# Performance work log

Hardware: AMD Instinct MI355X
Metric: run time of the kernel (lower is better)

## Reference

```python
import jax, jax.numpy as jnp
import numpy as np

B, S, D, H = 2, 2048, 1024, 16
DK = D // H


def setup_inputs() -> dict:
    key = jax.random.key(0)
    ks = jax.random.split(key, 12)
    scale = 1.0 / np.sqrt(D)
    inp = {
        "q": jax.random.normal(ks[0], (B, S, D), jnp.float32),
        "k": jax.random.normal(ks[1], (B, S, D), jnp.float32),
        "v": jax.random.normal(ks[2], (B, S, D), jnp.float32),
        "mask": jax.random.randint(ks[3], (B, 1, S, S), 0, 2, jnp.int32),
        "w_q": jax.random.normal(ks[4], (D, D), jnp.float32) * scale,
        "b_q": jnp.zeros((D,), jnp.float32),
        "w_k": jax.random.normal(ks[5], (D, D), jnp.float32) * scale,
        "b_k": jnp.zeros((D,), jnp.float32),
        "w_v": jax.random.normal(ks[6], (D, D), jnp.float32) * scale,
        "b_v": jnp.zeros((D,), jnp.float32),
        "w_o": jax.random.normal(ks[7], (D, D), jnp.float32) * scale,
        "b_o": jnp.zeros((D,), jnp.float32),
    }
    return inp


def reference(q, k, v, mask, w_q, b_q, w_k, b_k, w_v, b_v, w_o, b_o):
    # linear projections (torch Linear: x @ W.T + b)
    qp = q @ w_q.T + b_q  # [B,S,D]
    kp = k @ w_k.T + b_k
    vp = v @ w_v.T + b_v
    # split heads -> [B,H,S,DK]
    qh = qp.reshape(B, S, H, DK).transpose(0, 2, 1, 3)
    kh = kp.reshape(B, S, H, DK).transpose(0, 2, 1, 3)
    vh = vp.reshape(B, S, H, DK).transpose(0, 2, 1, 3)
    # scaled dot-product attention
    scores = jnp.einsum("bhqd,bhkd->bhqk", qh, kh) / jnp.sqrt(jnp.float32(DK))
    scores = jnp.where(mask == 0, jnp.float32(-1e9), scores)
    attn = jax.nn.softmax(scores, axis=-1)
    ctx = jnp.einsum("bhqk,bhkd->bhqd", attn, vh)  # [B,H,S,DK]
    ctx = ctx.transpose(0, 2, 1, 3).reshape(B, S, D)
    return ctx @ w_o.T + b_o
```

## Files before the change

### kernel.cpp

```cpp
#include <hip/hip_runtime.h>
#include <hip/hip_bf16.h>
#include <cstdint>

#define DEVINL __device__ __forceinline__

using bfrag = __attribute__((ext_vector_type(8))) __bf16;
using f32x4 = __attribute__((ext_vector_type(4))) float;
using f32x16 = __attribute__((ext_vector_type(16))) float;
using u16x4 = __attribute__((ext_vector_type(4))) unsigned short;
using u16x8 = __attribute__((ext_vector_type(8))) unsigned short;
using u32x4 = __attribute__((ext_vector_type(4))) unsigned int;

static constexpr int S_ = 2048;
static constexpr int D_ = 1024;
static constexpr int MROWS = 4096;

DEVINL unsigned short f2bf(float f) {
  __hip_bfloat16 h = __float2bfloat16(f);
  union { __hip_bfloat16 h; unsigned short u; } cv; cv.h = h; return cv.u;
}

DEVINL float fexp2(float x) {
#if __has_builtin(__builtin_amdgcn_exp2f)
  return __builtin_amdgcn_exp2f(x);
#else
  return exp2f(x);
#endif
}

DEVINL unsigned cvtpk(float lo, float hi) {
  unsigned r;
  asm("v_cvt_pk_bf16_f32 %0, %1, %2" : "=v"(r) : "v"(lo), "v"(hi));
  return r;
}

DEVINL void plswap(unsigned& x, unsigned& y) {
#if __has_builtin(__builtin_amdgcn_permlane32_swap)
  auto r = __builtin_amdgcn_permlane32_swap(x, y, false, false);
  x = r[0]; y = r[1];
#else
  unsigned px = __shfl_xor(x, 32), py = __shfl_xor(y, 32);
  bool h = (threadIdx.x & 32) != 0;
  unsigned nx = h ? py : x;
  unsigned ny = h ? y : px;
  x = nx; y = ny;
#endif
}

DEVINL void async_copy16(void* lds, const void* g) {
  __builtin_amdgcn_global_load_lds(
      (const __attribute__((address_space(1))) unsigned int*)g,
      (__attribute__((address_space(3))) unsigned int*)lds, 16, 0, 0);
}

struct CvtAll {
  const float* src[7];
  unsigned short* dst[7];
  int n4[7];
  const int* mask;
  unsigned long long* bits;
  int nmask;
};

__global__ __launch_bounds__(256) void cvt_all(CvtAll a) {
  if (blockIdx.y == 7) {
    const int n = a.nmask;
    for (int i = blockIdx.x * 256 + threadIdx.x; i < n; i += gridDim.x * 256) {
      unsigned long long b = __ballot(a.mask[i] != 0);
      if ((threadIdx.x & 63) == 0) a.bits[i >> 6] = b;
    }
    return;
  }
  const float* __restrict__ in = a.src[blockIdx.y];
  unsigned short* __restrict__ out = a.dst[blockIdx.y];
  const int n4 = a.n4[blockIdx.y];
  for (int i = blockIdx.x * 256 + threadIdx.x; i < n4; i += gridDim.x * 256) {
    f32x4 v = ((const f32x4*)in)[i];
    u16x4 o;
    o[0] = f2bf(v[0]); o[1] = f2bf(v[1]); o[2] = f2bf(v[2]); o[3] = f2bf(v[3]);
    ((u16x4*)out)[i] = o;
  }
}

template <int OMODE>
DEVINL void gemm_body(const unsigned short* __restrict__ A, const unsigned short* __restrict__ W,
                      const float* __restrict__ bias, void* __restrict__ Cout,
                      int K, int N, float oscale,
                      unsigned short* As, unsigned short* Bs, int m0, int n0) {
  const int t = threadIdx.x;
  const int lane = t & 63, wave = t >> 6;
  const int wr = wave >> 1, wc = wave & 1;
  const int g = lane >> 4, q = lane & 15;

  f32x4 acc[4][4] = {};

  const int srow = t >> 3;
  const int scol = (t & 7) * 8;
  const size_t abase = (size_t)(m0 + srow) * K + scol;
  const size_t bbase = (size_t)(n0 + srow) * K + scol;
  char* AsB = (char*)As;
  char* BsB = (char*)Bs;

  for (int k0 = 0; k0 < K; k0 += 64) {
    __syncthreads();
#pragma unroll
    for (int c = 0; c < 4; ++c) {
      async_copy16(AsB + c * 4096 + wave * 1024, A + abase + (size_t)c * 32 * K + k0);
      async_copy16(BsB + c * 4096 + wave * 1024, W + bbase + (size_t)c * 32 * K + k0);
    }
    __syncthreads();
#pragma unroll
    for (int kk = 0; kk < 64; kk += 32) {
      bfrag af[4], bf[4];
#pragma unroll
      for (int i = 0; i < 4; ++i)
        af[i] = *reinterpret_cast<const bfrag*>(&As[(wr * 64 + i * 16 + q) * 64 + kk + g * 8]);
#pragma unroll
      for (int j = 0; j < 4; ++j)
        bf[j] = *reinterpret_cast<const bfrag*>(&Bs[(wc * 64 + j * 16 + q) * 64 + kk + g * 8]);
#pragma unroll
      for (int i = 0; i < 4; ++i)
#pragma unroll
        for (int j = 0; j < 4; ++j)
          acc[i][j] = __builtin_amdgcn_mfma_f32_16x16x32_bf16(af[i], bf[j], acc[i][j], 0, 0, 0);
    }
  }

  float bv[4];
#pragma unroll
  for (int j = 0; j < 4; ++j) bv[j] = bias[n0 + wc * 64 + j * 16 + q];
#pragma unroll
  for (int i = 0; i < 4; ++i)
#pragma unroll
    for (int j = 0; j < 4; ++j) {
      int rowb = m0 + wr * 64 + i * 16 + g * 4;
      int col = n0 + wc * 64 + j * 16 + q;
      if (OMODE == 2) {
        u16x4 o;
#pragma unroll
        for (int r = 0; r < 4; ++r) o[r] = f2bf(acc[i][j][r] + bv[j]);
        *reinterpret_cast<u16x4*>(&((unsigned short*)Cout)[(size_t)col * MROWS + rowb]) = o;
      } else {
#pragma unroll
        for (int r = 0; r < 4; ++r) {
          float val = (acc[i][j][r] + bv[j]) * oscale;
          if (OMODE == 1)
            ((float*)Cout)[(size_t)(rowb + r) * N + col] = val;
          else
            ((unsigned short*)Cout)[(size_t)(rowb + r) * N + col] = f2bf(val);
        }
      }
    }
}

__global__ __launch_bounds__(256, 2) void qkv_gemm(const unsigned short* __restrict__ Abase,
                                                   const unsigned short* __restrict__ Wbase,
                                                   const float* __restrict__ b_q,
                                                   const float* __restrict__ b_k,
                                                   const float* __restrict__ b_v,
                                                   unsigned short* __restrict__ Qp,
                                                   unsigned short* __restrict__ Kp,
                                                   unsigned short* __restrict__ VpT) {
  __shared__ unsigned short As[128 * 64];
  __shared__ unsigned short Bs[128 * 64];
  const int lin = blockIdx.x + 8 * (blockIdx.y + 32 * blockIdx.z);
  const int tile = (lin & 7) * 96 + (lin >> 3);
  const int bx = tile & 7, by = (tile >> 3) & 31, z = tile >> 8;
  const unsigned short* A = Abase + (size_t)z * MROWS * D_;
  const unsigned short* W = Wbase + (size_t)z * D_ * D_;
  const int m0 = by * 128, n0 = bx * 128;
  if (z == 2) {
    gemm_body<2>(A, W, b_v, VpT, D_, D_, 1.0f, As, Bs, m0, n0);
  } else if (z == 1) {
    gemm_body<0>(A, W, b_k, Kp, D_, D_, 1.0f, As, Bs, m0, n0);
  } else {
    gemm_body<0>(A, W, b_q, Qp, D_, D_, 0.125f * 1.44269504088896340736f, As, Bs, m0, n0);
  }
}

__global__ __launch_bounds__(256, 2) void out_gemm(const unsigned short* __restrict__ A,
                                                   const unsigned short* __restrict__ W,
                                                   const float* __restrict__ bias,
                                                   float* __restrict__ out) {
  __shared__ unsigned short As[128 * 64];
  __shared__ unsigned short Bs[128 * 64];
  const int lin = blockIdx.x + 8 * blockIdx.y;
  const int tile = (lin & 7) * 32 + (lin >> 3);
  const int bx = tile & 7, by = tile >> 3;
  gemm_body<1>(A, W, bias, out, D_, D_, 1.0f, As, Bs, by * 128, bx * 128);
}

__global__ __launch_bounds__(256, 2) void attn_kernel(const unsigned short* __restrict__ Qp,
                                                      const unsigned short* __restrict__ Kp,
                                                      const unsigned short* __restrict__ VpT,
                                                      const unsigned int* __restrict__ mbits32,
                                                      unsigned short* __restrict__ ctx) {
  __shared__ unsigned short Ks[2][128 * 64];
  __shared__ unsigned short Vt[2][64 * 128];

  const int t = threadIdx.x, lane = t & 63, wave = t >> 6;
  const int hi = lane >> 5, qh = lane & 31;
  const int h = blockIdx.y, b = blockIdx.z;
  const int q0 = blockIdx.x * 128;
  const int qrow = q0 + wave * 32 + qh;

  const size_t qoff = ((size_t)b * S_ + qrow) * D_ + h * 64;
  bfrag qf[4];
#pragma unroll
  for (int ks = 0; ks < 4; ++ks)
    qf[ks] = *reinterpret_cast<const bfrag*>(&Qp[qoff + ks * 16 + hi * 8]);

  f32x16 acc_o[2] = {};
  f32x16 acc_l = {};

  u16x8 onesv;
#pragma unroll
  for (int j = 0; j < 8; ++j) onesv[j] = 0x3F80;
  const bfrag ones = __builtin_bit_cast(bfrag, onesv);

  const int krow = wave * 8 + (lane >> 3);
  const int ksc = ((lane & 7) ^ (lane >> 3)) * 8;
  const size_t kbase = (size_t)b * S_ * D_ + (size_t)h * 64;
  const int vrow = wave * 4 + (lane >> 4);
  const int vsc = ((lane & 15) ^ (vrow & 7)) * 8;
  const size_t vtrow0 = (size_t)h * 64;
  const size_t vtcol0 = (size_t)b * S_;

  char* KsB = (char*)&Ks[0][0];
  char* VtB = (char*)&Vt[0][0];
  const unsigned int* mrow = mbits32 + ((size_t)b * S_ + qrow) * (S_ / 32);
  const int swz = qh & 7;

  constexpr int NT = S_ / 128;

  auto stage = [&](int buf, int ti) {
#pragma unroll
    for (int c = 0; c < 4; ++c)
      async_copy16(KsB + buf * 16384 + c * 4096 + wave * 1024,
                   &Kp[kbase + (size_t)(ti * 128 + c * 32 + krow) * D_ + ksc]);
#pragma unroll
    for (int c = 0; c < 4; ++c)
      async_copy16(VtB + buf * 16384 + c * 4096 + wave * 1024,
                   &VpT[(vtrow0 + c * 16 + vrow) * MROWS + vtcol0 + ti * 128 + vsc]);
  };

  stage(0, 0);
  __syncthreads();

  auto tile_body = [&](int ti, int cur) {
    const int nxt = cur ^ 1;
    if (ti + 1 < NT) stage(nxt, ti + 1);
    u32x4 m4 = *reinterpret_cast<const u32x4*>(mrow + ti * 4);

    f32x16 sc[4];
    const f32x16 fz = {};
    __builtin_amdgcn_s_setprio(1);
#pragma unroll
    for (int kb = 0; kb < 4; ++kb) {
#pragma unroll
      for (int ks = 0; ks < 4; ++ks) {
        bfrag kf = *reinterpret_cast<const bfrag*>(
            KsB + cur * 16384 + (kb * 32 + qh) * 128 + ((((2 * ks + hi) ^ swz) & 7) << 4));
        sc[kb] = __builtin_amdgcn_mfma_f32_32x32x16_bf16(kf, qf[ks], ks == 0 ? fz : sc[kb], 0, 0, 0);
      }
    }
    __builtin_amdgcn_s_setprio(0);

    const int sh4 = 4 * hi;
#pragma unroll
    for (int kb = 0; kb < 4; ++kb) {
      unsigned w = m4[kb] >> sh4;
#pragma unroll
      for (int g2 = 0; g2 < 4; ++g2) {
        unsigned nib = (w >> (8 * g2)) & 0xFu;
#pragma unroll
        for (int r3 = 0; r3 < 4; ++r3) {
          float p = fexp2(sc[kb][g2 * 4 + r3]);
          sc[kb][g2 * 4 + r3] = (nib & (1u << r3)) ? p : 0.f;
        }
      }
    }

    bfrag pa[8];
#pragma unroll
    for (int ks = 0; ks < 8; ++ks) {
      const int o = ks * 8;
      unsigned a1 = cvtpk(sc[(o + 0) >> 4][(o + 0) & 15], sc[(o + 1) >> 4][(o + 1) & 15]);
      unsigned a2 = cvtpk(sc[(o + 2) >> 4][(o + 2) & 15], sc[(o + 3) >> 4][(o + 3) & 15]);
      unsigned b1 = cvtpk(sc[(o + 4) >> 4][(o + 4) & 15], sc[(o + 5) >> 4][(o + 5) & 15]);
      unsigned b2 = cvtpk(sc[(o + 6) >> 4][(o + 6) & 15], sc[(o + 7) >> 4][(o + 7) & 15]);
      plswap(a1, b1);
      plswap(a2, b2);
      u32x4 wv; wv[0] = a1; wv[1] = a2; wv[2] = b1; wv[3] = b2;
      pa[ks] = __builtin_bit_cast(bfrag, wv);
    }

    __builtin_amdgcn_s_setprio(1);
#pragma unroll
    for (int ks = 0; ks < 8; ++ks) {
      acc_l = __builtin_amdgcn_mfma_f32_32x32x16_bf16(ones, pa[ks], acc_l, 0, 0, 0);
#pragma unroll
      for (int dblk = 0; dblk < 2; ++dblk) {
        bfrag va = *reinterpret_cast<const bfrag*>(
            VtB + cur * 16384 + (dblk * 32 + qh) * 256 + ((((2 * ks + hi) ^ swz) & 15) << 4));
        acc_o[dblk] = __builtin_amdgcn_mfma_f32_32x32x16_bf16(va, pa[ks], acc_o[dblk], 0, 0, 0);
      }
    }
    __builtin_amdgcn_s_setprio(0);
    __syncthreads();
  };

#pragma unroll 1
  for (int ti = 0; ti < NT; ti += 2) {
    tile_body(ti, 0);
    tile_body(ti + 1, 1);
  }

  float inv = 1.f / acc_l[0];
#pragma unroll
  for (int dblk = 0; dblk < 2; ++dblk)
#pragma unroll
    for (int g2 = 0; g2 < 4; ++g2) {
      u16x4 o;
#pragma unroll
      for (int r3 = 0; r3 < 4; ++r3) o[r3] = f2bf(acc_o[dblk][g2 * 4 + r3] * inv);
      int d0 = dblk * 32 + 8 * g2 + 4 * hi;
      *reinterpret_cast<u16x4*>(&ctx[((size_t)b * S_ + qrow) * D_ + h * 64 + d0]) = o;
    }
}

extern "C" void kernel_launch(void* const* d_in, const int* in_sizes, int n_in,
                              void* d_out, int out_size, void* d_ws, size_t ws_size,
                              hipStream_t stream) {
  const float* q = (const float*)d_in[0];
  const float* k = (const float*)d_in[1];
  const float* v = (const float*)d_in[2];
  const int* mask = (const int*)d_in[3];
  const float* w_q = (const float*)d_in[4];
  const float* b_q = (const float*)d_in[5];
  const float* w_k = (const float*)d_in[6];
  const float* b_k = (const float*)d_in[7];
  const float* w_v = (const float*)d_in[8];
  const float* b_v = (const float*)d_in[9];
  const float* w_o = (const float*)d_in[10];
  const float* b_o = (const float*)d_in[11];
  float* out = (float*)d_out;

  char* ws = (char*)d_ws;
  const size_t SZ_IN = (size_t)MROWS * D_ * 2;
  const size_t SZ_W = (size_t)D_ * D_ * 2;
  unsigned short* qb = (unsigned short*)(ws + 0);
  unsigned short* wqb = (unsigned short*)(ws + 3 * SZ_IN);
  unsigned short* wob = (unsigned short*)(ws + 3 * SZ_IN + 3 * SZ_W);
  unsigned short* Qp = (unsigned short*)(ws + 3 * SZ_IN + 4 * SZ_W);
  unsigned short* ctx = (unsigned short*)(ws + 6 * SZ_IN + 4 * SZ_W);
  unsigned long long* mbits = (unsigned long long*)(ws + 7 * SZ_IN + 4 * SZ_W);
  unsigned short* kb = qb + MROWS * D_;
  unsigned short* vb = kb + MROWS * D_;
  unsigned short* wkb = wqb + D_ * D_;
  unsigned short* wvb = wkb + D_ * D_;
  unsigned short* Kp = Qp + MROWS * D_;
  unsigned short* VpT = Kp + MROWS * D_;

  CvtAll ca;
  ca.src[0] = q;   ca.dst[0] = qb;  ca.n4[0] = MROWS * D_ / 4;
  ca.src[1] = k;   ca.dst[1] = kb;  ca.n4[1] = MROWS * D_ / 4;
  ca.src[2] = v;   ca.dst[2] = vb;  ca.n4[2] = MROWS * D_ / 4;
  ca.src[3] = w_q; ca.dst[3] = wqb; ca.n4[3] = D_ * D_ / 4;
  ca.src[4] = w_k; ca.dst[4] = wkb; ca.n4[4] = D_ * D_ / 4;
  ca.src[5] = w_v; ca.dst[5] = wvb; ca.n4[5] = D_ * D_ / 4;
  ca.src[6] = w_o; ca.dst[6] = wob; ca.n4[6] = D_ * D_ / 4;
  ca.mask = mask; ca.bits = mbits; ca.nmask = 2 * S_ * S_;
  cvt_all<<<dim3(2048, 8), 256, 0, stream>>>(ca);

  qkv_gemm<<<dim3(D_ / 128, MROWS / 128, 3), 256, 0, stream>>>(qb, wqb, b_q, b_k, b_v,
                                                               Qp, Kp, VpT);

  attn_kernel<<<dim3(S_ / 128, 16, 2), 256, 0, stream>>>(Qp, Kp, VpT,
                                                         (const unsigned int*)mbits, ctx);

  out_gemm<<<dim3(D_ / 128, MROWS / 128), 256, 0, stream>>>(ctx, wob, b_o, out);
}
```

Baseline: 136.3 us.

## Fuse fp32-to-bf16 activation conversion into QKV GEMM A-tile loads

The separate pass that converted the q/k/v activations to bf16 is removed. The QKV GEMM now reads fp32 activations directly, converts them in registers and writes bf16 into LDS. This drops a full write and re-read of about 24MB of bf16 intermediates, at the cost of synchronous register loads in place of async LDS copies for the A tile, and twice the A-side bytes per tile. The attention grid is also remapped with a swizzled tile order to improve cache locality across heads.

Measured after the change: 136.2 us. Within noise of the previous version (-0.0%).

```diff
diff --git a/kernel.cpp b/kernel.cpp
--- a/kernel.cpp
+++ b/kernel.cpp
@@ -53,17 +53,16 @@
       (__attribute__((address_space(3))) unsigned int*)lds, 16, 0, 0);
 }
 
-struct CvtAll {
-  const float* src[7];
-  unsigned short* dst[7];
-  int n4[7];
+struct CvtW {
+  const float* src[4];
+  unsigned short* dst[4];
   const int* mask;
   unsigned long long* bits;
   int nmask;
 };
 
-__global__ __launch_bounds__(256) void cvt_all(CvtAll a) {
-  if (blockIdx.y == 7) {
+__global__ __launch_bounds__(256) void cvt_w(CvtW a) {
+  if (blockIdx.y == 4) {
     const int n = a.nmask;
     for (int i = blockIdx.x * 256 + threadIdx.x; i < n; i += gridDim.x * 256) {
       unsigned long long b = __ballot(a.mask[i] != 0);
@@ -73,7 +72,7 @@
   }
   const float* __restrict__ in = a.src[blockIdx.y];
   unsigned short* __restrict__ out = a.dst[blockIdx.y];
-  const int n4 = a.n4[blockIdx.y];
+  const int n4 = D_ * D_ / 4;
   for (int i = blockIdx.x * 256 + threadIdx.x; i < n4; i += gridDim.x * 256) {
     f32x4 v = ((const f32x4*)in)[i];
     u16x4 o;
@@ -82,8 +81,8 @@
   }
 }
 
-template <int OMODE>
-DEVINL void gemm_body(const unsigned short* __restrict__ A, const unsigned short* __restrict__ W,
+template <int OMODE, bool AF32>
+DEVINL void gemm_body(const void* __restrict__ Ap, const unsigned short* __restrict__ W,
                       const float* __restrict__ bias, void* __restrict__ Cout,
                       int K, int N, float oscale,
                       unsigned short* As, unsigned short* Bs, int m0, int n0) {
@@ -96,7 +95,6 @@
 
   const int srow = t >> 3;
   const int scol = (t & 7) * 8;
-  const size_t abase = (size_t)(m0 + srow) * K + scol;
   const size_t bbase = (size_t)(n0 + srow) * K + scol;
   char* AsB = (char*)As;
   char* BsB = (char*)Bs;
@@ -104,9 +102,30 @@
   for (int k0 = 0; k0 < K; k0 += 64) {
     __syncthreads();
 #pragma unroll
-    for (int c = 0; c < 4; ++c) {
-      async_copy16(AsB + c * 4096 + wave * 1024, A + abase + (size_t)c * 32 * K + k0);
+    for (int c = 0; c < 4; ++c)
       async_copy16(BsB + c * 4096 + wave * 1024, W + bbase + (size_t)c * 32 * K + k0);
+    if (AF32) {
+      const float* Af = (const float*)Ap;
+      f32x4 v0[4], v1[4];
+#pragma unroll
+      for (int i = 0; i < 4; ++i) {
+        const float* src = Af + (size_t)(m0 + (t >> 3) + i * 32) * K + k0 + (t & 7) * 8;
+        v0[i] = *reinterpret_cast<const f32x4*>(src);
+        v1[i] = *reinterpret_cast<const f32x4*>(src + 4);
+      }
+#pragma unroll
+      for (int i = 0; i < 4; ++i) {
+        u16x8 o;
+#pragma unroll
+        for (int j = 0; j < 4; ++j) { o[j] = f2bf(v0[i][j]); o[4 + j] = f2bf(v1[i][j]); }
+        *reinterpret_cast<u16x8*>(AsB + ((t >> 3) + i * 32) * 128 + (t & 7) * 16) = o;
+      }
+    } else {
+      const unsigned short* Ab = (const unsigned short*)Ap;
+#pragma unroll
+      for (int c = 0; c < 4; ++c)
+        async_copy16(AsB + c * 4096 + wave * 1024,
+                     Ab + (size_t)(m0 + srow + c * 32) * K + scol + k0);
     }
     __syncthreads();
 #pragma unroll
@@ -153,7 +172,9 @@
     }
 }
 
-__global__ __launch_bounds__(256, 2) void qkv_gemm(const unsigned short* __restrict__ Abase,
+__global__ __launch_bounds__(256, 2) void qkv_gemm(const float* __restrict__ Aq,
+                                                   const float* __restrict__ Ak,
+                                                   const float* __restrict__ Av,
                                                    const unsigned short* __restrict__ Wbase,
                                                    const float* __restrict__ b_q,
                                                    const float* __restrict__ b_k,
@@ -166,15 +187,14 @@
   const int lin = blockIdx.x + 8 * (blockIdx.y + 32 * blockIdx.z);
   const int tile = (lin & 7) * 96 + (lin >> 3);
   const int bx = tile & 7, by = (tile >> 3) & 31, z = tile >> 8;
-  const unsigned short* A = Abase + (size_t)z * MROWS * D_;
   const unsigned short* W = Wbase + (size_t)z * D_ * D_;
   const int m0 = by * 128, n0 = bx * 128;
   if (z == 2) {
-    gemm_body<2>(A, W, b_v, VpT, D_, D_, 1.0f, As, Bs, m0, n0);
+    gemm_body<2, true>(Av, W, b_v, VpT, D_, D_, 1.0f, As, Bs, m0, n0);
   } else if (z == 1) {
-    gemm_body<0>(A, W, b_k, Kp, D_, D_, 1.0f, As, Bs, m0, n0);
+    gemm_body<0, true>(Ak, W, b_k, Kp, D_, D_, 1.0f, As, Bs, m0, n0);
   } else {
-    gemm_body<0>(A, W, b_q, Qp, D_, D_, 0.125f * 1.44269504088896340736f, As, Bs, m0, n0);
+    gemm_body<0, true>(Aq, W, b_q, Qp, D_, D_, 0.125f * 1.44269504088896340736f, As, Bs, m0, n0);
   }
 }
 
@@ -187,7 +207,7 @@
   const int lin = blockIdx.x + 8 * blockIdx.y;
   const int tile = (lin & 7) * 32 + (lin >> 3);
   const int bx = tile & 7, by = tile >> 3;
-  gemm_body<1>(A, W, bias, out, D_, D_, 1.0f, As, Bs, by * 128, bx * 128);
+  gemm_body<1, false>(A, W, bias, out, D_, D_, 1.0f, As, Bs, by * 128, bx * 128);
 }
 
 __global__ __launch_bounds__(256, 2) void attn_kernel(const unsigned short* __restrict__ Qp,
@@ -200,8 +220,11 @@
 
   const int t = threadIdx.x, lane = t & 63, wave = t >> 6;
   const int hi = lane >> 5, qh = lane & 31;
-  const int h = blockIdx.y, b = blockIdx.z;
-  const int q0 = blockIdx.x * 128;
+  const int id = blockIdx.x + 16 * (blockIdx.y + 16 * blockIdx.z);
+  const int tile = (id & 7) * 64 + (id >> 3);
+  const int qt = tile & 15, bh = tile >> 4;
+  const int h = bh & 15, b = bh >> 4;
+  const int q0 = qt * 128;
   const int qrow = q0 + wave * 32 + qh;
 
   const size_t qoff = ((size_t)b * S_ + qrow) * D_ + h * 64;
@@ -349,31 +372,25 @@
   char* ws = (char*)d_ws;
   const size_t SZ_IN = (size_t)MROWS * D_ * 2;
   const size_t SZ_W = (size_t)D_ * D_ * 2;
-  unsigned short* qb = (unsigned short*)(ws + 0);
   unsigned short* wqb = (unsigned short*)(ws + 3 * SZ_IN);
   unsigned short* wob = (unsigned short*)(ws + 3 * SZ_IN + 3 * SZ_W);
   unsigned short* Qp = (unsigned short*)(ws + 3 * SZ_IN + 4 * SZ_W);
   unsigned short* ctx = (unsigned short*)(ws + 6 * SZ_IN + 4 * SZ_W);
   unsigned long long* mbits = (unsigned long long*)(ws + 7 * SZ_IN + 4 * SZ_W);
-  unsigned short* kb = qb + MROWS * D_;
-  unsigned short* vb = kb + MROWS * D_;
   unsigned short* wkb = wqb + D_ * D_;
   unsigned short* wvb = wkb + D_ * D_;
   unsigned short* Kp = Qp + MROWS * D_;
   unsigned short* VpT = Kp + MROWS * D_;
 
-  CvtAll ca;
-  ca.src[0] = q;   ca.dst[0] = qb;  ca.n4[0] = MROWS * D_ / 4;
-  ca.src[1] = k;   ca.dst[1] = kb;  ca.n4[1] = MROWS * D_ / 4;
-  ca.src[2] = v;   ca.dst[2] = vb;  ca.n4[2] = MROWS * D_ / 4;
-  ca.src[3] = w_q; ca.dst[3] = wqb; ca.n4[3] = D_ * D_ / 4;
-  ca.src[4] = w_k; ca.dst[4] = wkb; ca.n4[4] = D_ * D_ / 4;
-  ca.src[5] = w_v; ca.dst[5] = wvb; ca.n4[5] = D_ * D_ / 4;
-  ca.src[6] = w_o; ca.dst[6] = wob; ca.n4[6] = D_ * D_ / 4;
-  ca.mask = mask; ca.bits = mbits; ca.nmask = 2 * S_ * S_;
-  cvt_all<<<dim3(2048, 8), 256, 0, stream>>>(ca);
-
-  qkv_gemm<<<dim3(D_ / 128, MROWS / 128, 3), 256, 0, stream>>>(qb, wqb, b_q, b_k, b_v,
+  CvtW cw;
+  cw.src[0] = w_q; cw.dst[0] = wqb;
+  cw.src[1] = w_k; cw.dst[1] = wkb;
+  cw.src[2] = w_v; cw.dst[2] = wvb;
+  cw.src[3] = w_o; cw.dst[3] = wob;
+  cw.mask = mask; cw.bits = mbits; cw.nmask = 2 * S_ * S_;
+  cvt_w<<<dim3(1024, 5), 256, 0, stream>>>(cw);
+
+  qkv_gemm<<<dim3(D_ / 128, MROWS / 128, 3), 256, 0, stream>>>(q, k, v, wqb, b_q, b_k, b_v,
                                                                Qp, Kp, VpT);
 
   attn_kernel<<<dim3(S_ / 128, 16, 2), 256, 0, stream>>>(Qp, Kp, VpT,
```
